# Kernel optimization log

Hardware: AMD Instinct MI355X
Metric: run time of the kernel (lower is better)

Reference implementation:

```python
import jax, jax.numpy as jnp
import numpy as np

H = 8  # num_heads
EPS = 1e-5


def _lin_params(key, din, dout, scale=0.02):
    kw, _ = jax.random.split(key)
    W = jax.random.normal(kw, (din, dout), jnp.float32) * scale
    b = jnp.zeros((dout,), jnp.float32)
    return W, b


def _edge_attention(x_src, x_dst, ei, ea, Wq, bq, Wk, bk, Wv, bv, We, be, Wo, bo, n_dst):
    out_c = Wq.shape[1]
    D = out_c // H
    scale = D ** -0.5
    q = (x_dst @ Wq + bq).reshape(-1, H, D)
    k = (x_src @ Wk + bk).reshape(-1, H, D)
    v = (x_src @ Wv + bv).reshape(-1, H, D)
    e = (ea @ We + be).reshape(-1, H, D)
    src, dst = ei[0], ei[1]
    ke = k[src] + e                                # [E,H,D]
    ve = v[src] + e                                # [E,H,D]
    s = jnp.einsum('ehd,ehd->eh', q[dst], ke) * scale  # [E,H]
    # segment (per-destination) softmax, numerically stable
    m = jax.ops.segment_max(s, dst, num_segments=n_dst)
    ex = jnp.exp(s - m[dst])
    den = jax.ops.segment_sum(ex, dst, num_segments=n_dst)
    a = ex / den[dst]                              # [E,H]  (dropout = identity in eval)
    agg = jax.ops.segment_sum(a[..., None] * ve, dst, num_segments=n_dst)  # [N_dst,H,D]
    return agg.reshape(n_dst, out_c) @ Wo + bo


def _layernorm(x, g, b):
    mu = jnp.mean(x, axis=-1, keepdims=True)
    var = jnp.mean((x - mu) ** 2, axis=-1, keepdims=True)
    return (x - mu) * jax.lax.rsqrt(var + EPS) * g + b


def setup_inputs() -> dict:
    key = jax.random.key(0)
    ks = jax.random.split(key, 32)
    N_pc, N_gr, E_pp, E_pg = 50000, 8000, 400000, 100000
    din, dout, de = 128, 128, 64
    inp = {}
    inp['x_pc'] = jax.random.normal(ks[0], (N_pc, din), jnp.float32)
    inp['x_gr'] = jax.random.normal(ks[1], (N_gr, din), jnp.float32)
    inp['ea_pp'] = jax.random.normal(ks[2], (E_pp, de), jnp.float32)
    inp['ea_pg'] = jax.random.normal(ks[3], (E_pg, de), jnp.float32)
    inp['ei_pp'] = jax.random.randint(ks[4], (2, E_pp), 0, N_pc, jnp.int32)
    src_pg = jax.random.randint(ks[5], (E_pg,), 0, N_pc, jnp.int32)
    dst_pg = jax.random.randint(ks[6], (E_pg,), 0, N_gr, jnp.int32)
    inp['ei_pg'] = jnp.stack([src_pg, dst_pg])
    i = 7
    for et in ('pp', 'pg'):
        for nm, d_in in (('Wq', din), ('Wk', din), ('Wv', din), ('We', de), ('Wo', dout)):
            W, b = _lin_params(ks[i], d_in, dout); i += 1
            inp[f'{nm}_{et}'] = W
            inp[f'b{nm[1].lower()}_{et}'] = b
    for nt, d_in in (('pc', din), ('gr', din)):
        W, b = _lin_params(ks[i], d_in, dout); i += 1
        inp[f'Wnp_{nt}'] = W
        inp[f'bnp_{nt}'] = b
        inp[f'g_{nt}'] = jnp.ones((dout,), jnp.float32)
        inp[f'bln_{nt}'] = jnp.zeros((dout,), jnp.float32)
    return inp


def reference(x_pc, x_gr, ea_pp, ea_pg, ei_pp, ei_pg,
              Wq_pp, bq_pp, Wk_pp, bk_pp, Wv_pp, bv_pp, We_pp, be_pp, Wo_pp, bo_pp,
              Wq_pg, bq_pg, Wk_pg, bk_pg, Wv_pg, bv_pg, We_pg, be_pg, Wo_pg, bo_pg,
              Wnp_pc, bnp_pc, Wnp_gr, bnp_gr, g_pc, bln_pc, g_gr, bln_gr):
    N_pc, N_gr = x_pc.shape[0], x_gr.shape[0]
    out_pc = x_pc @ Wnp_pc + bnp_pc
    out_gr = x_gr @ Wnp_gr + bnp_gr
    out_pc = out_pc + _edge_attention(x_pc, x_pc, ei_pp, ea_pp,
                                      Wq_pp, bq_pp, Wk_pp, bk_pp, Wv_pp, bv_pp,
                                      We_pp, be_pp, Wo_pp, bo_pp, N_pc)
    out_gr = out_gr + _edge_attention(x_pc, x_gr, ei_pg, ea_pg,
                                      Wq_pg, bq_pg, Wk_pg, bk_pg, Wv_pg, bv_pg,
                                      We_pg, be_pg, Wo_pg, bo_pg, N_gr)
    out_pc = _layernorm(out_pc, g_pc, bln_pc)
    out_gr = _layernorm(out_gr, g_gr, bln_gr)
    return out_pc, out_gr
```

## Files before the change

### kernel.cpp

```cpp
#include <hip/hip_runtime.h>
#include <hip/hip_bf16.h>
#include <stdint.h>

typedef short short8 __attribute__((ext_vector_type(8)));
typedef float f32x4 __attribute__((ext_vector_type(4)));

__device__ __forceinline__ unsigned short f2bf(float x) {
    unsigned u = __float_as_uint(x);
    u += 0x7fffu + ((u >> 16) & 1u);
    return (unsigned short)(u >> 16);
}
__device__ __forceinline__ float bflo(unsigned u) { return __uint_as_float(u << 16); }
__device__ __forceinline__ float bfhi(unsigned u) { return __uint_as_float(u & 0xffff0000u); }

struct WDesc { const float* src; unsigned short* dst; int K, ldd, koff, perm; };
struct WPack { WDesc w[12]; };

__global__ __launch_bounds__(256) void prep_and_count(WPack p,
        const int* __restrict__ d0, int E0, int* c0,
        const int* __restrict__ d1, int E1, int* c1, int nPrep) {
    if ((int)blockIdx.x < nPrep) {
        int wi = blockIdx.x >> 2, chunk = blockIdx.x & 3;
        WDesc d = p.w[wi];
        int total = d.K * 128, cs = total >> 2;
        int lo = chunk * cs, hi = lo + cs;
        for (int i = lo + threadIdx.x; i < hi; i += 256) {
            int n = i / d.K, k = i - n * d.K;
            int kk = d.perm ? (2 * (k & 63) + (k >> 6)) : k;
            d.dst[(size_t)n * d.ldd + d.koff + kk] = f2bf(d.src[(size_t)k * 128 + n]);
        }
    } else {
        int t = (blockIdx.x - nPrep) * 256 + threadIdx.x;
        if (t < E0) atomicAdd(&c0[d0[t]], 1);
        else if (t < E0 + E1) atomicAdd(&c1[d1[t - E0]], 1);
    }
}

struct NodeOut { const unsigned short* Wt; const float* bias; unsigned int* out; int ldc, coloff; };
struct NodePack { NodeOut d[5]; int nout; };

__global__ __launch_bounds__(256) void gemm_node(const float* __restrict__ A0, int M0, NodePack p0,
                                                 int B0,
                                                 const float* __restrict__ A1, int M1, NodePack p1) {
    constexpr int K = 128, LDA = 136, LDB = 72, TLD = 133;
    __shared__ __align__(16) unsigned short As[64 * LDA];
    __shared__ __align__(16) unsigned short Bs[128 * LDB];

    const float* A; int M; NodePack dp; int blk;
    if ((int)blockIdx.x < B0) { A = A0; M = M0; dp = p0; blk = blockIdx.x; }
    else { A = A1; M = M1; dp = p1; blk = blockIdx.x - B0; }

    const int tid = threadIdx.x;
    const int rbase = blk * 64;

    for (int slot = tid; slot < 64 * 16; slot += 256) {
        int row = slot >> 4, kg = slot & 15;
        int gr = rbase + row;
        short8 s8 = {0, 0, 0, 0, 0, 0, 0, 0};
        if (gr < M) {
            const float* a = A + (size_t)gr * K + kg * 8;
            float4 f0 = *reinterpret_cast<const float4*>(a);
            float4 f1 = *reinterpret_cast<const float4*>(a + 4);
            s8[0] = (short)f2bf(f0.x); s8[1] = (short)f2bf(f0.y);
            s8[2] = (short)f2bf(f0.z); s8[3] = (short)f2bf(f0.w);
            s8[4] = (short)f2bf(f1.x); s8[5] = (short)f2bf(f1.y);
            s8[6] = (short)f2bf(f1.z); s8[7] = (short)f2bf(f1.w);
        }
        *reinterpret_cast<short8*>(&As[row * LDA + kg * 8]) = s8;
    }

    const int lane = tid & 63, w = tid >> 6;
    const int rb = (w >> 1) * 32, cb = (w & 1) * 64;
    const int qd = lane >> 4, l16 = lane & 15;

    for (int o = 0; o < dp.nout; ++o) {
        NodeOut d = dp.d[o];
        f32x4 acc[2][4];
#pragma unroll
        for (int rt = 0; rt < 2; ++rt)
#pragma unroll
            for (int ct = 0; ct < 4; ++ct) { f32x4 z = {0.f,0.f,0.f,0.f}; acc[rt][ct] = z; }

        for (int kc = 0; kc < K; kc += 64) {
            __syncthreads();
            for (int slot = tid; slot < 128 * 8; slot += 256) {
                int n = slot >> 3, kg = slot & 7;
                *reinterpret_cast<short8*>(&Bs[n * LDB + kg * 8]) =
                    *reinterpret_cast<const short8*>(d.Wt + (size_t)n * K + kc + kg * 8);
            }
            __syncthreads();
#pragma unroll
            for (int ks = 0; ks < 64; ks += 32) {
                short8 af[2], bfr[4];
#pragma unroll
                for (int rt = 0; rt < 2; ++rt)
                    af[rt] = *reinterpret_cast<const short8*>(
                        &As[(rb + rt * 16 + l16) * LDA + kc + ks + qd * 8]);
#pragma unroll
                for (int ct = 0; ct < 4; ++ct)
                    bfr[ct] = *reinterpret_cast<const short8*>(
                        &Bs[(cb + ct * 16 + l16) * LDB + ks + qd * 8]);
#pragma unroll
                for (int rt = 0; rt < 2; ++rt)
#pragma unroll
                    for (int ct = 0; ct < 4; ++ct)
                        acc[rt][ct] = __builtin_amdgcn_mfma_f32_16x16x32_bf16(
                            af[rt], bfr[ct], acc[rt][ct], 0, 0, 0);
            }
        }

        __syncthreads();
        unsigned short* tile = Bs;
#pragma unroll
        for (int ct = 0; ct < 4; ++ct) {
            int col = cb + ct * 16 + l16;
            float bv = d.bias[col];
#pragma unroll
            for (int rt = 0; rt < 2; ++rt)
#pragma unroll
                for (int r = 0; r < 4; ++r)
                    tile[(rb + rt * 16 + qd * 4 + r) * TLD + col] = f2bf(acc[rt][ct][r] + bv);
        }
        __syncthreads();
#pragma unroll
        for (int rep = 0; rep < 4; ++rep) {
            int lrow = (tid >> 4) + rep * 16, seg = tid & 15;
            int gr = rbase + lrow;
            if (gr < M) {
                uint4 pk;
#pragma unroll
                for (int j = 0; j < 4; ++j) {
                    int pcol = seg * 4 + j;
                    unsigned lo16 = tile[lrow * TLD + pcol];
                    unsigned hi16 = tile[lrow * TLD + pcol + 64];
                    ((unsigned*)&pk)[j] = lo16 | (hi16 << 16);
                }
                *reinterpret_cast<uint4*>(&d.out[(size_t)gr * d.ldc + d.coloff + seg * 4]) = pk;
            }
        }
    }
}

struct EdgePack {
    const float* A; const unsigned short* Wt; const float* bias;
    const int* pos; unsigned int* out; int M;
};

__global__ __launch_bounds__(256) void gemm_edge(EdgePack p0, EdgePack p1, int B0) {
    constexpr int K = 64, LDA = 72, LDB = 72, TLD = 133;
    __shared__ __align__(16) unsigned short As[64 * LDA];
    __shared__ __align__(16) unsigned short Bs[128 * LDB];

    EdgePack p; int blk;
    if ((int)blockIdx.x < B0) { p = p0; blk = blockIdx.x; } else { p = p1; blk = blockIdx.x - B0; }

    const int tid = threadIdx.x;
    const int rbase = blk * 64;

    for (int slot = tid; slot < 64 * 8; slot += 256) {
        int row = slot >> 3, kg = slot & 7;
        int gr = rbase + row;
        short8 s8 = {0, 0, 0, 0, 0, 0, 0, 0};
        if (gr < p.M) {
            const float* a = p.A + (size_t)gr * K + kg * 8;
            float4 f0 = *reinterpret_cast<const float4*>(a);
            float4 f1 = *reinterpret_cast<const float4*>(a + 4);
            s8[0] = (short)f2bf(f0.x); s8[1] = (short)f2bf(f0.y);
            s8[2] = (short)f2bf(f0.z); s8[3] = (short)f2bf(f0.w);
            s8[4] = (short)f2bf(f1.x); s8[5] = (short)f2bf(f1.y);
            s8[6] = (short)f2bf(f1.z); s8[7] = (short)f2bf(f1.w);
        }
        *reinterpret_cast<short8*>(&As[row * LDA + kg * 8]) = s8;
    }
    for (int slot = tid; slot < 128 * 8; slot += 256) {
        int n = slot >> 3, kg = slot & 7;
        *reinterpret_cast<short8*>(&Bs[n * LDB + kg * 8]) =
            *reinterpret_cast<const short8*>(p.Wt + (size_t)n * K + kg * 8);
    }
    __syncthreads();

    const int lane = tid & 63, w = tid >> 6;
    const int rb = (w >> 1) * 32, cb = (w & 1) * 64;
    const int qd = lane >> 4, l16 = lane & 15;

    f32x4 acc[2][4];
#pragma unroll
    for (int rt = 0; rt < 2; ++rt)
#pragma unroll
        for (int ct = 0; ct < 4; ++ct) { f32x4 z = {0.f,0.f,0.f,0.f}; acc[rt][ct] = z; }

#pragma unroll
    for (int ks = 0; ks < 64; ks += 32) {
        short8 af[2], bfr[4];
#pragma unroll
        for (int rt = 0; rt < 2; ++rt)
            af[rt] = *reinterpret_cast<const short8*>(&As[(rb + rt * 16 + l16) * LDA + ks + qd * 8]);
#pragma unroll
        for (int ct = 0; ct < 4; ++ct)
            bfr[ct] = *reinterpret_cast<const short8*>(&Bs[(cb + ct * 16 + l16) * LDB + ks + qd * 8]);
#pragma unroll
        for (int rt = 0; rt < 2; ++rt)
#pragma unroll
            for (int ct = 0; ct < 4; ++ct)
                acc[rt][ct] = __builtin_amdgcn_mfma_f32_16x16x32_bf16(
                    af[rt], bfr[ct], acc[rt][ct], 0, 0, 0);
    }

    __syncthreads();
    unsigned short* tile = Bs;
#pragma unroll
    for (int ct = 0; ct < 4; ++ct) {
        int col = cb + ct * 16 + l16;
        float bv = p.bias[col];
#pragma unroll
        for (int rt = 0; rt < 2; ++rt)
#pragma unroll
            for (int r = 0; r < 4; ++r)
                tile[(rb + rt * 16 + qd * 4 + r) * TLD + col] = f2bf(acc[rt][ct][r] + bv);
    }
    __syncthreads();
#pragma unroll
    for (int rep = 0; rep < 4; ++rep) {
        int lrow = (tid >> 4) + rep * 16, seg = tid & 15;
        int gr = rbase + lrow;
        if (gr < p.M) {
            int dpos = p.pos[gr];
            uint4 pk;
#pragma unroll
            for (int j = 0; j < 4; ++j) {
                int pcol = seg * 4 + j;
                unsigned lo16 = tile[lrow * TLD + pcol];
                unsigned hi16 = tile[lrow * TLD + pcol + 64];
                ((unsigned*)&pk)[j] = lo16 | (hi16 << 16);
            }
            *reinterpret_cast<uint4*>(&p.out[(size_t)dpos * 64 + seg * 4]) = pk;
        }
    }
}

struct OutPack {
    const unsigned short* Aagg; const float* Ax;
    const unsigned short* Wt;
    const float *bo, *bnp, *g, *bln; float* out; int M;
};

__global__ __launch_bounds__(256) void gemm_out_ln(OutPack p0, OutPack p1, int B0) {
    constexpr int K = 256, LDA = 264, LDB = 72, FTLD = 132;
    __shared__ __align__(16) char smemA[64 * LDA * 2];
    __shared__ __align__(16) unsigned short Bs[128 * LDB];
    unsigned short* As = (unsigned short*)smemA;

    OutPack p; int blk;
    if ((int)blockIdx.x < B0) { p = p0; blk = blockIdx.x; } else { p = p1; blk = blockIdx.x - B0; }

    const int tid = threadIdx.x;
    const int rbase = blk * 64;

    for (int slot = tid; slot < 64 * 32; slot += 256) {
        int row = slot >> 5, kg = slot & 31;
        int gr = rbase + row;
        short8 s8 = {0, 0, 0, 0, 0, 0, 0, 0};
        if (gr < p.M) {
            if (kg < 16) {
                s8 = *reinterpret_cast<const short8*>(p.Aagg + (size_t)gr * 128 + kg * 8);
            } else {
                const float* a = p.Ax + (size_t)gr * 128 + (kg - 16) * 8;
                float4 f0 = *reinterpret_cast<const float4*>(a);
                float4 f1 = *reinterpret_cast<const float4*>(a + 4);
                s8[0] = (short)f2bf(f0.x); s8[1] = (short)f2bf(f0.y);
                s8[2] = (short)f2bf(f0.z); s8[3] = (short)f2bf(f0.w);
                s8[4] = (short)f2bf(f1.x); s8[5] = (short)f2bf(f1.y);
                s8[6] = (short)f2bf(f1.z); s8[7] = (short)f2bf(f1.w);
            }
        }
        *reinterpret_cast<short8*>(&As[row * LDA + kg * 8]) = s8;
    }

    const int lane = tid & 63, w = tid >> 6;
    const int rb = (w >> 1) * 32, cb = (w & 1) * 64;
    const int qd = lane >> 4, l16 = lane & 15;

    f32x4 acc[2][4];
#pragma unroll
    for (int rt = 0; rt < 2; ++rt)
#pragma unroll
        for (int ct = 0; ct < 4; ++ct) { f32x4 z = {0.f,0.f,0.f,0.f}; acc[rt][ct] = z; }

    for (int kc = 0; kc < K; kc += 64) {
        __syncthreads();
        for (int slot = tid; slot < 128 * 8; slot += 256) {
            int n = slot >> 3, kg = slot & 7;
            *reinterpret_cast<short8*>(&Bs[n * LDB + kg * 8]) =
                *reinterpret_cast<const short8*>(p.Wt + (size_t)n * K + kc + kg * 8);
        }
        __syncthreads();
#pragma unroll
        for (int ks = 0; ks < 64; ks += 32) {
            short8 af[2], bfr[4];
#pragma unroll
            for (int rt = 0; rt < 2; ++rt)
                af[rt] = *reinterpret_cast<const short8*>(
                    &As[(rb + rt * 16 + l16) * LDA + kc + ks + qd * 8]);
#pragma unroll
            for (int ct = 0; ct < 4; ++ct)
                bfr[ct] = *reinterpret_cast<const short8*>(
                    &Bs[(cb + ct * 16 + l16) * LDB + ks + qd * 8]);
#pragma unroll
            for (int rt = 0; rt < 2; ++rt)
#pragma unroll
                for (int ct = 0; ct < 4; ++ct)
                    acc[rt][ct] = __builtin_amdgcn_mfma_f32_16x16x32_bf16(
                        af[rt], bfr[ct], acc[rt][ct], 0, 0, 0);
        }
    }

    __syncthreads();
    float* ftile = (float*)smemA;
#pragma unroll
    for (int ct = 0; ct < 4; ++ct) {
        int col = cb + ct * 16 + l16;
        float bv = p.bo[col] + p.bnp[col];
#pragma unroll
        for (int rt = 0; rt < 2; ++rt)
#pragma unroll
            for (int r = 0; r < 4; ++r)
                ftile[(rb + rt * 16 + qd * 4 + r) * FTLD + col] = acc[rt][ct][r] + bv;
    }
    __syncthreads();

    int r = tid >> 2, q4 = tid & 3;
    const float* rowp = &ftile[r * FTLD + q4 * 32];
    float s = 0.f, sq = 0.f;
#pragma unroll
    for (int j = 0; j < 8; ++j) {
        float4 v = *reinterpret_cast<const float4*>(rowp + j * 4);
        s += v.x + v.y + v.z + v.w;
        sq += v.x * v.x + v.y * v.y + v.z * v.z + v.w * v.w;
    }
    s += __shfl_xor(s, 1, 64);  s += __shfl_xor(s, 2, 64);
    sq += __shfl_xor(sq, 1, 64); sq += __shfl_xor(sq, 2, 64);
    float mu = s * (1.f / 128.f);
    float var = sq * (1.f / 128.f) - mu * mu;
    float rs = rsqrtf(var + 1e-5f);
    int gr = rbase + r;
    if (gr < p.M) {
#pragma unroll
        for (int j = 0; j < 8; ++j) {
            float4 v = *reinterpret_cast<const float4*>(rowp + j * 4);
            int c = q4 * 32 + j * 4;
            float4 gg = *reinterpret_cast<const float4*>(p.g + c);
            float4 bb = *reinterpret_cast<const float4*>(p.bln + c);
            float4 o;
            o.x = (v.x - mu) * rs * gg.x + bb.x;
            o.y = (v.y - mu) * rs * gg.y + bb.y;
            o.z = (v.z - mu) * rs * gg.z + bb.z;
            o.w = (v.w - mu) * rs * gg.w + bb.w;
            *reinterpret_cast<float4*>(&p.out[(size_t)gr * 128 + c]) = o;
        }
    }
}

__global__ __launch_bounds__(1024) void scan_partial(const int* c0, int N0, int* rp0, int* bs0, int B0,
                                                     const int* c1, int N1, int* rp1, int* bs1) {
    __shared__ int wsum[16];
    const int* c; int* rp; int* bs; int N; int blk;
    if ((int)blockIdx.x < B0) { c = c0; rp = rp0; bs = bs0; N = N0; blk = blockIdx.x; }
    else { c = c1; rp = rp1; bs = bs1; N = N1; blk = blockIdx.x - B0; }
    int tid = threadIdx.x, lane = tid & 63, w = tid >> 6;
    int i = blk * 1024 + tid;
    int v = (i < N) ? c[i] : 0;
    int s = v;
#pragma unroll
    for (int off = 1; off < 64; off <<= 1) {
        int t = __shfl_up(s, off, 64);
        if (lane >= off) s += t;
    }
    if (lane == 63) wsum[w] = s;
    __syncthreads();
    if (w == 0 && lane < 16) {
        int ws = wsum[lane];
#pragma unroll
        for (int off = 1; off < 16; off <<= 1) {
            int t = __shfl_up(ws, off, 64);
            if (lane >= off) ws += t;
        }
        wsum[lane] = ws;
    }
    __syncthreads();
    int wexcl = (w == 0) ? 0 : wsum[w - 1];
    if (i < N) rp[i] = wexcl + s - v;
    if (tid == 0) bs[blk] = wsum[15];
}

__global__ __launch_bounds__(128) void scan_mid(const int* bs0, int* off0, int B0, int* rpN0,
                                                const int* bs1, int* off1, int B1, int* rpN1) {
    int w = threadIdx.x >> 6, lane = threadIdx.x & 63;
    const int* bs = w ? bs1 : bs0;
    int* off = w ? off1 : off0;
    int B = w ? B1 : B0;
    int* rpN = w ? rpN1 : rpN0;
    int v = (lane < B) ? bs[lane] : 0;
    int s = v;
#pragma unroll
    for (int o = 1; o < 64; o <<= 1) {
        int t = __shfl_up(s, o, 64);
        if (lane >= o) s += t;
    }
    if (lane < B) off[lane] = s - v;
    int total = __shfl(s, B - 1, 64);
    if (lane == 0) *rpN = total;
}

__global__ __launch_bounds__(1024) void scan_add(int* rp0, int* cur0, const int* off0, int N0, int B0,
                                                 int* rp1, int* cur1, const int* off1, int N1) {
    int* rp; int* cur; const int* off; int N; int blk;
    if ((int)blockIdx.x < B0) { rp = rp0; cur = cur0; off = off0; N = N0; blk = blockIdx.x; }
    else { rp = rp1; cur = cur1; off = off1; N = N1; blk = blockIdx.x - B0; }
    int i = blk * 1024 + threadIdx.x;
    if (i < N) {
        int vv = rp[i] + off[blk];
        rp[i] = vv;
        cur[i] = vv;
    }
}

__global__ __launch_bounds__(256) void scatter_both(
    const int* __restrict__ s0, const int* __restrict__ d0, int E0, int* cur0, int* pos0, int* srcs0,
    const int* __restrict__ s1, const int* __restrict__ d1, int E1, int* cur1, int* pos1, int* srcs1) {
    int t = blockIdx.x * 256 + threadIdx.x;
    if (t < E0) {
        int p = atomicAdd(&cur0[d0[t]], 1);
        pos0[t] = p;
        srcs0[p] = s0[t];
    } else if (t < E0 + E1) {
        int tt = t - E0;
        int p = atomicAdd(&cur1[d1[tt]], 1);
        pos1[tt] = p;
        srcs1[p] = s1[tt];
    }
}

struct AttnPack {
    const unsigned int *q, *kv, *e;
    const int *srcs;
    const int *row_ptr;
    unsigned int* agg; int N;
};

__global__ __launch_bounds__(256) void attn_gather(AttnPack a0, AttnPack a1, int B0) {
    AttnPack a; int blk;
    if ((int)blockIdx.x < B0) { a = a0; blk = blockIdx.x; } else { a = a1; blk = blockIdx.x - B0; }
    int dst = blk * 4 + (threadIdx.x >> 6);
    if (dst >= a.N) return;
    int lane = threadIdx.x & 63;

    unsigned qp = a.q[(size_t)dst * 64 + lane];
    float qlo = bflo(qp), qhi = bfhi(qp);
    int beg = a.row_ptr[dst], end = a.row_ptr[dst + 1];
    float denl = 0.f, denh = 0.f, accl = 0.f, acch = 0.f;

    int sC = a.srcs[beg];
    unsigned kC = a.kv[(size_t)sC * 128 + lane];
    unsigned vC = a.kv[(size_t)sC * 128 + 64 + lane];
    unsigned eC = a.e[(size_t)beg * 64 + lane];

    for (int i = beg; i < end; ++i) {
        int sN = a.srcs[i + 1];
        unsigned kN = a.kv[(size_t)sN * 128 + lane];
        unsigned vN = a.kv[(size_t)sN * 128 + 64 + lane];
        unsigned eN = a.e[(size_t)(i + 1) * 64 + lane];

        float kl = bflo(kC), kh = bfhi(kC);
        float vl = bflo(vC), vh = bfhi(vC);
        float el = bflo(eC), eh = bfhi(eC);
        float pl = qlo * (kl + el), ph = qhi * (kh + eh);
#pragma unroll
        for (int m = 1; m < 16; m <<= 1) {
            pl += __shfl_xor(pl, m, 64);
            ph += __shfl_xor(ph, m, 64);
        }
        float exl = __expf(pl * 0.25f), exh = __expf(ph * 0.25f);
        denl += exl; denh += exh;
        accl += exl * (vl + el);
        acch += exh * (vh + eh);
        kC = kN; vC = vN; eC = eN;
    }
    float ol = denl > 0.f ? accl / denl : 0.f;
    float oh = denh > 0.f ? acch / denh : 0.f;
    a.agg[(size_t)dst * 64 + lane] = (unsigned)f2bf(ol) | ((unsigned)f2bf(oh) << 16);
}

extern "C" void kernel_launch(void* const* d_in, const int* in_sizes, int n_in,
                              void* d_out, int out_size, void* d_ws, size_t ws_size,
                              hipStream_t stream) {
    const float* x_pc  = (const float*)d_in[0];
    const float* x_gr  = (const float*)d_in[1];
    const float* ea_pp = (const float*)d_in[2];
    const float* ea_pg = (const float*)d_in[3];
    const int* ei_pp   = (const int*)d_in[4];
    const int* ei_pg   = (const int*)d_in[5];
    const float *Wq_pp = (const float*)d_in[6],  *bq_pp = (const float*)d_in[7];
    const float *Wk_pp = (const float*)d_in[8],  *bk_pp = (const float*)d_in[9];
    const float *Wv_pp = (const float*)d_in[10], *bv_pp = (const float*)d_in[11];
    const float *We_pp = (const float*)d_in[12], *be_pp = (const float*)d_in[13];
    const float *Wo_pp = (const float*)d_in[14], *bo_pp = (const float*)d_in[15];
    const float *Wq_pg = (const float*)d_in[16], *bq_pg = (const float*)d_in[17];
    const float *Wk_pg = (const float*)d_in[18], *bk_pg = (const float*)d_in[19];
    const float *Wv_pg = (const float*)d_in[20], *bv_pg = (const float*)d_in[21];
    const float *We_pg = (const float*)d_in[22], *be_pg = (const float*)d_in[23];
    const float *Wo_pg = (const float*)d_in[24], *bo_pg = (const float*)d_in[25];
    const float *Wnp_pc = (const float*)d_in[26], *bnp_pc = (const float*)d_in[27];
    const float *g_pc   = (const float*)d_in[28], *bln_pc = (const float*)d_in[29];
    const float *Wnp_gr = (const float*)d_in[30], *bnp_gr = (const float*)d_in[31];
    const float *g_gr   = (const float*)d_in[32], *bln_gr = (const float*)d_in[33];

    const int N_pc = in_sizes[0] / 128;
    const int N_gr = in_sizes[1] / 128;
    const int E_pp = in_sizes[4] / 2;
    const int E_pg = in_sizes[5] / 2;

    char* ws = (char*)d_ws;
    size_t off = 0;
    auto alloc = [&](size_t bytes) -> char* {
        char* p = ws + off;
        off += (bytes + 255) & ~(size_t)255;
        return p;
    };
    unsigned short* Wt_q_pp = (unsigned short*)alloc(128 * 128 * 2);
    unsigned short* Wt_k_pp = (unsigned short*)alloc(128 * 128 * 2);
    unsigned short* Wt_v_pp = (unsigned short*)alloc(128 * 128 * 2);
    unsigned short* Wt_k_pg = (unsigned short*)alloc(128 * 128 * 2);
    unsigned short* Wt_v_pg = (unsigned short*)alloc(128 * 128 * 2);
    unsigned short* Wt_q_pg = (unsigned short*)alloc(128 * 128 * 2);
    unsigned short* Wt_e_pp = (unsigned short*)alloc(64 * 128 * 2);
    unsigned short* Wt_e_pg = (unsigned short*)alloc(64 * 128 * 2);
    unsigned short* Wt_cat_pp = (unsigned short*)alloc(256 * 128 * 2);
    unsigned short* Wt_cat_gr = (unsigned short*)alloc(256 * 128 * 2);

    unsigned int* q_pp  = (unsigned int*)alloc((size_t)N_pc * 64 * 4);
    unsigned int* kv_pp = (unsigned int*)alloc((size_t)N_pc * 128 * 4);
    unsigned int* q_pg  = (unsigned int*)alloc((size_t)N_gr * 64 * 4);
    unsigned int* kv_pg = (unsigned int*)alloc((size_t)N_pc * 128 * 4);
    unsigned int* e_pp  = (unsigned int*)alloc((size_t)(E_pp + 1) * 64 * 4);
    unsigned int* e_pg  = (unsigned int*)alloc((size_t)(E_pg + 1) * 64 * 4);
    unsigned int* agg_pp = (unsigned int*)alloc((size_t)N_pc * 64 * 4);
    unsigned int* agg_pg = (unsigned int*)alloc((size_t)N_gr * 64 * 4);
    int* row_ptr_pp = (int*)alloc((size_t)(N_pc + 1) * 4);
    int* cursor_pp  = (int*)alloc((size_t)N_pc * 4);
    int* pos_pp     = (int*)alloc((size_t)E_pp * 4);
    int* row_ptr_pg = (int*)alloc((size_t)(N_gr + 1) * 4);
    int* cursor_pg  = (int*)alloc((size_t)N_gr * 4);
    int* pos_pg     = (int*)alloc((size_t)E_pg * 4);
    int* bsum_pp    = (int*)alloc(64 * 4);
    int* boff_pp    = (int*)alloc(64 * 4);
    int* bsum_pg    = (int*)alloc(64 * 4);
    int* boff_pg    = (int*)alloc(64 * 4);
    char* zbase = ws + off;
    int* counts_pp = (int*)alloc((size_t)N_pc * 4);
    int* counts_pg = (int*)alloc((size_t)N_gr * 4);
    int* srcs_pp   = (int*)alloc((size_t)(E_pp + 8) * 4);
    int* srcs_pg   = (int*)alloc((size_t)(E_pg + 8) * 4);
    size_t zbytes = (size_t)((ws + off) - zbase);
    hipMemsetAsync(zbase, 0, zbytes, stream);

    float* out_pc = (float*)d_out;
    float* out_gr = out_pc + (size_t)N_pc * 128;

    const int* src_pp = ei_pp;
    const int* dst_pp = ei_pp + E_pp;
    const int* src_pg = ei_pg;
    const int* dst_pg = ei_pg + E_pg;

    WPack wp;
    wp.w[0]  = {Wq_pp, Wt_q_pp, 128, 128, 0, 0};
    wp.w[1]  = {Wk_pp, Wt_k_pp, 128, 128, 0, 0};
    wp.w[2]  = {Wv_pp, Wt_v_pp, 128, 128, 0, 0};
    wp.w[3]  = {Wk_pg, Wt_k_pg, 128, 128, 0, 0};
    wp.w[4]  = {Wv_pg, Wt_v_pg, 128, 128, 0, 0};
    wp.w[5]  = {Wq_pg, Wt_q_pg, 128, 128, 0, 0};
    wp.w[6]  = {We_pp, Wt_e_pp, 64, 64, 0, 0};
    wp.w[7]  = {We_pg, Wt_e_pg, 64, 64, 0, 0};
    wp.w[8]  = {Wo_pp, Wt_cat_pp, 128, 256, 0, 1};
    wp.w[9]  = {Wnp_pc, Wt_cat_pp, 128, 256, 128, 0};
    wp.w[10] = {Wo_pg, Wt_cat_gr, 128, 256, 0, 1};
    wp.w[11] = {Wnp_gr, Wt_cat_gr, 128, 256, 128, 0};
    const int NPREP = 48;
    const int gE = (E_pp + E_pg + 255) / 256;
    prep_and_count<<<NPREP + gE, 256, 0, stream>>>(wp, dst_pp, E_pp, counts_pp,
                                                   dst_pg, E_pg, counts_pg, NPREP);

    const int Bs_pp = (N_pc + 1023) / 1024, Bs_pg = (N_gr + 1023) / 1024;
    scan_partial<<<Bs_pp + Bs_pg, 1024, 0, stream>>>(counts_pp, N_pc, row_ptr_pp, bsum_pp, Bs_pp,
                                                     counts_pg, N_gr, row_ptr_pg, bsum_pg);
    scan_mid<<<1, 128, 0, stream>>>(bsum_pp, boff_pp, Bs_pp, &row_ptr_pp[N_pc],
                                    bsum_pg, boff_pg, Bs_pg, &row_ptr_pg[N_gr]);
    scan_add<<<Bs_pp + Bs_pg, 1024, 0, stream>>>(row_ptr_pp, cursor_pp, boff_pp, N_pc, Bs_pp,
                                                 row_ptr_pg, cursor_pg, boff_pg, N_gr);
    scatter_both<<<gE, 256, 0, stream>>>(src_pp, dst_pp, E_pp, cursor_pp, pos_pp, srcs_pp,
                                         src_pg, dst_pg, E_pg, cursor_pg, pos_pg, srcs_pg);

    NodePack np;
    np.d[0] = {Wt_q_pp, bq_pp, q_pp, 64, 0};
    np.d[1] = {Wt_k_pp, bk_pp, kv_pp, 128, 0};
    np.d[2] = {Wt_v_pp, bv_pp, kv_pp, 128, 64};
    np.d[3] = {Wt_k_pg, bk_pg, kv_pg, 128, 0};
    np.d[4] = {Wt_v_pg, bv_pg, kv_pg, 128, 64};
    np.nout = 5;
    NodePack ng{};
    ng.d[0] = {Wt_q_pg, bq_pg, q_pg, 64, 0};
    ng.nout = 1;
    int Bn0 = (N_pc + 63) / 64, Bn1 = (N_gr + 63) / 64;
    gemm_node<<<Bn0 + Bn1, 256, 0, stream>>>(x_pc, N_pc, np, Bn0, x_gr, N_gr, ng);

    EdgePack ep0 = {ea_pp, Wt_e_pp, be_pp, pos_pp, e_pp, E_pp};
    EdgePack ep1 = {ea_pg, Wt_e_pg, be_pg, pos_pg, e_pg, E_pg};
    int Be0 = (E_pp + 63) / 64, Be1 = (E_pg + 63) / 64;
    gemm_edge<<<Be0 + Be1, 256, 0, stream>>>(ep0, ep1, Be0);

    AttnPack ap0 = {q_pp, kv_pp, e_pp, srcs_pp, row_ptr_pp, agg_pp, N_pc};
    AttnPack ap1 = {q_pg, kv_pg, e_pg, srcs_pg, row_ptr_pg, agg_pg, N_gr};
    int Ba0 = (N_pc + 3) / 4, Ba1 = (N_gr + 3) / 4;
    attn_gather<<<Ba0 + Ba1, 256, 0, stream>>>(ap0, ap1, Ba0);

    OutPack op0 = {(const unsigned short*)agg_pp, x_pc, Wt_cat_pp, bo_pp, bnp_pc, g_pc, bln_pc, out_pc, N_pc};
    OutPack op1 = {(const unsigned short*)agg_pg, x_gr, Wt_cat_gr, bo_pg, bnp_gr, g_gr, bln_gr, out_gr, N_gr};
    int Bo0 = (N_pc + 63) / 64, Bo1 = (N_gr + 63) / 64;
    gemm_out_ln<<<Bo0 + Bo1, 256, 0, stream>>>(op0, op1, Bo0);
}
```

Baseline: 532.8 us.

## Fuse CSR scatter into edge GEMM, single-pass lookback scan, merge node/edge GEMMs

Replaces the three-kernel scan with a single decoupled-lookback scan kernel and drops the separate scatter kernel. The edge GEMM now does the atomic cursor increments itself, keeping positions in shared memory instead of a global pos array. Node and edge GEMMs are merged into one launch, and srcs now stores pre-multiplied offsets so the attention kernel skips that multiply, which also gets vectorised f32x2 math. This cuts launches and global traffic. The risk is that the lookback spin-waits assume all earlier blocks are resident, and atomic ordering makes edge order within each segment nondeterministic.

```diff
diff --git a/kernel.cpp b/kernel.cpp
--- a/kernel.cpp
+++ b/kernel.cpp
@@ -4,14 +4,19 @@
 
 typedef short short8 __attribute__((ext_vector_type(8)));
 typedef float f32x4 __attribute__((ext_vector_type(4)));
+typedef float f32x2 __attribute__((ext_vector_type(2)));
 
 __device__ __forceinline__ unsigned short f2bf(float x) {
     unsigned u = __float_as_uint(x);
     u += 0x7fffu + ((u >> 16) & 1u);
     return (unsigned short)(u >> 16);
 }
-__device__ __forceinline__ float bflo(unsigned u) { return __uint_as_float(u << 16); }
-__device__ __forceinline__ float bfhi(unsigned u) { return __uint_as_float(u & 0xffff0000u); }
+__device__ __forceinline__ f32x2 up2(unsigned u) {
+    f32x2 r;
+    r.x = __uint_as_float(u << 16);
+    r.y = __uint_as_float(u & 0xffff0000u);
+    return r;
+}
 
 struct WDesc { const float* src; unsigned short* dst; int K, ldd, koff, perm; };
 struct WPack { WDesc w[12]; };
@@ -36,85 +41,145 @@
     }
 }
 
+__global__ __launch_bounds__(1024) void scan_lookback(
+        const int* c0, int N0, int* rp0, int* cur0, int B0, int* flg0,
+        const int* c1, int N1, int* rp1, int* cur1, int* flg1) {
+    __shared__ int wsum[16];
+    __shared__ int pref_s;
+    const int* c; int* rp; int* cur; int* flg; int N, blk, B;
+    if ((int)blockIdx.x < B0) { c = c0; rp = rp0; cur = cur0; flg = flg0; N = N0; blk = blockIdx.x; B = B0; }
+    else { c = c1; rp = rp1; cur = cur1; flg = flg1; N = N1; blk = blockIdx.x - B0; B = gridDim.x - B0; }
+    int tid = threadIdx.x, lane = tid & 63, w = tid >> 6;
+    int i = blk * 1024 + tid;
+    int v = (i < N) ? c[i] : 0;
+    int s = v;
+#pragma unroll
+    for (int off = 1; off < 64; off <<= 1) {
+        int t = __shfl_up(s, off, 64);
+        if (lane >= off) s += t;
+    }
+    if (lane == 63) wsum[w] = s;
+    __syncthreads();
+    if (w == 0 && lane < 16) {
+        int ws = wsum[lane];
+#pragma unroll
+        for (int off = 1; off < 16; off <<= 1) {
+            int t = __shfl_up(ws, off, 64);
+            if (lane >= off) ws += t;
+        }
+        wsum[lane] = ws;
+    }
+    __syncthreads();
+    int total = wsum[15];
+    if (tid == 0) atomicExch(&flg[blk], total + 1);
+    if (w == 0) {
+        int mysum = 0;
+        if (lane < blk) {
+            int t;
+            do { t = atomicAdd(&flg[lane], 0); } while (t == 0);
+            mysum = t - 1;
+        }
+#pragma unroll
+        for (int o = 1; o < 64; o <<= 1) mysum += __shfl_xor(mysum, o, 64);
+        if (lane == 0) pref_s = mysum;
+    }
+    __syncthreads();
+    int prefix = pref_s;
+    int wexcl = (w == 0) ? 0 : wsum[w - 1];
+    if (i < N) {
+        int val = prefix + wexcl + (s - v);
+        rp[i] = val;
+        cur[i] = val;
+    }
+    if (blk == B - 1 && tid == 0) rp[N] = prefix + total;
+}
+
 struct NodeOut { const unsigned short* Wt; const float* bias; unsigned int* out; int ldc, coloff; };
 struct NodePack { NodeOut d[5]; int nout; };
-
-__global__ __launch_bounds__(256) void gemm_node(const float* __restrict__ A0, int M0, NodePack p0,
-                                                 int B0,
-                                                 const float* __restrict__ A1, int M1, NodePack p1) {
-    constexpr int K = 128, LDA = 136, LDB = 72, TLD = 133;
-    __shared__ __align__(16) unsigned short As[64 * LDA];
-    __shared__ __align__(16) unsigned short Bs[128 * LDB];
-
-    const float* A; int M; NodePack dp; int blk;
-    if ((int)blockIdx.x < B0) { A = A0; M = M0; dp = p0; blk = blockIdx.x; }
-    else { A = A1; M = M1; dp = p1; blk = blockIdx.x - B0; }
+struct EdgeJob {
+    const float* A; const unsigned short* Wt; const float* bias;
+    const int* srcI; const int* dstI; int* cursor; int* srcs; unsigned int* out; int M;
+};
+
+__global__ __launch_bounds__(256) void gemm_fused(
+        EdgeJob e0, EdgeJob e1, int Be0, int BeTot,
+        const float* An0, int Mn0, NodePack np0, int Bn0,
+        const float* An1, int Mn1, NodePack np1) {
+    __shared__ __align__(16) unsigned short sA[64 * 136];
+    __shared__ __align__(16) unsigned short sB[128 * 72];
+    __shared__ int pos_s[64];
 
     const int tid = threadIdx.x;
-    const int rbase = blk * 64;
-
-    for (int slot = tid; slot < 64 * 16; slot += 256) {
-        int row = slot >> 4, kg = slot & 15;
-        int gr = rbase + row;
-        short8 s8 = {0, 0, 0, 0, 0, 0, 0, 0};
-        if (gr < M) {
-            const float* a = A + (size_t)gr * K + kg * 8;
-            float4 f0 = *reinterpret_cast<const float4*>(a);
-            float4 f1 = *reinterpret_cast<const float4*>(a + 4);
-            s8[0] = (short)f2bf(f0.x); s8[1] = (short)f2bf(f0.y);
-            s8[2] = (short)f2bf(f0.z); s8[3] = (short)f2bf(f0.w);
-            s8[4] = (short)f2bf(f1.x); s8[5] = (short)f2bf(f1.y);
-            s8[6] = (short)f2bf(f1.z); s8[7] = (short)f2bf(f1.w);
-        }
-        *reinterpret_cast<short8*>(&As[row * LDA + kg * 8]) = s8;
-    }
-
     const int lane = tid & 63, w = tid >> 6;
     const int rb = (w >> 1) * 32, cb = (w & 1) * 64;
     const int qd = lane >> 4, l16 = lane & 15;
 
-    for (int o = 0; o < dp.nout; ++o) {
-        NodeOut d = dp.d[o];
+    if ((int)blockIdx.x < BeTot) {
+        constexpr int LDA = 72, LDB = 72, TLD = 133;
+        EdgeJob p; int blk;
+        if ((int)blockIdx.x < Be0) { p = e0; blk = blockIdx.x; }
+        else { p = e1; blk = blockIdx.x - Be0; }
+        const int rbase = blk * 64;
+
+        if (tid < 64) {
+            int t = rbase + tid, pp = 0;
+            if (t < p.M) {
+                int d = p.dstI[t];
+                pp = atomicAdd(&p.cursor[d], 1);
+                p.srcs[pp] = p.srcI[t] * 128;
+            }
+            pos_s[tid] = pp;
+        }
+        for (int slot = tid; slot < 64 * 8; slot += 256) {
+            int row = slot >> 3, kg = slot & 7;
+            int gr = rbase + row;
+            short8 s8 = {0, 0, 0, 0, 0, 0, 0, 0};
+            if (gr < p.M) {
+                const float* a = p.A + (size_t)gr * 64 + kg * 8;
+                float4 f0 = *reinterpret_cast<const float4*>(a);
+                float4 f1 = *reinterpret_cast<const float4*>(a + 4);
+                s8[0] = (short)f2bf(f0.x); s8[1] = (short)f2bf(f0.y);
+                s8[2] = (short)f2bf(f0.z); s8[3] = (short)f2bf(f0.w);
+                s8[4] = (short)f2bf(f1.x); s8[5] = (short)f2bf(f1.y);
+                s8[6] = (short)f2bf(f1.z); s8[7] = (short)f2bf(f1.w);
+            }
+            *reinterpret_cast<short8*>(&sA[row * LDA + kg * 8]) = s8;
+        }
+        for (int slot = tid; slot < 128 * 8; slot += 256) {
+            int n = slot >> 3, kg = slot & 7;
+            *reinterpret_cast<short8*>(&sB[n * LDB + kg * 8]) =
+                *reinterpret_cast<const short8*>(p.Wt + (size_t)n * 64 + kg * 8);
+        }
+        __syncthreads();
+
         f32x4 acc[2][4];
 #pragma unroll
         for (int rt = 0; rt < 2; ++rt)
 #pragma unroll
             for (int ct = 0; ct < 4; ++ct) { f32x4 z = {0.f,0.f,0.f,0.f}; acc[rt][ct] = z; }
-
-        for (int kc = 0; kc < K; kc += 64) {
-            __syncthreads();
-            for (int slot = tid; slot < 128 * 8; slot += 256) {
-                int n = slot >> 3, kg = slot & 7;
-                *reinterpret_cast<short8*>(&Bs[n * LDB + kg * 8]) =
-                    *reinterpret_cast<const short8*>(d.Wt + (size_t)n * K + kc + kg * 8);
-            }
-            __syncthreads();
-#pragma unroll
-            for (int ks = 0; ks < 64; ks += 32) {
-                short8 af[2], bfr[4];
-#pragma unroll
-                for (int rt = 0; rt < 2; ++rt)
-                    af[rt] = *reinterpret_cast<const short8*>(
-                        &As[(rb + rt * 16 + l16) * LDA + kc + ks + qd * 8]);
+#pragma unroll
+        for (int ks = 0; ks < 64; ks += 32) {
+            short8 af[2], bfr[4];
+#pragma unroll
+            for (int rt = 0; rt < 2; ++rt)
+                af[rt] = *reinterpret_cast<const short8*>(&sA[(rb + rt * 16 + l16) * LDA + ks + qd * 8]);
+#pragma unroll
+            for (int ct = 0; ct < 4; ++ct)
+                bfr[ct] = *reinterpret_cast<const short8*>(&sB[(cb + ct * 16 + l16) * LDB + ks + qd * 8]);
+#pragma unroll
+            for (int rt = 0; rt < 2; ++rt)
 #pragma unroll
                 for (int ct = 0; ct < 4; ++ct)
-                    bfr[ct] = *reinterpret_cast<const short8*>(
-                        &Bs[(cb + ct * 16 + l16) * LDB + ks + qd * 8]);
-#pragma unroll
-                for (int rt = 0; rt < 2; ++rt)
-#pragma unroll
-                    for (int ct = 0; ct < 4; ++ct)
-                        acc[rt][ct] = __builtin_amdgcn_mfma_f32_16x16x32_bf16(
-                            af[rt], bfr[ct], acc[rt][ct], 0, 0, 0);
-            }
+                    acc[rt][ct] = __builtin_amdgcn_mfma_f32_16x16x32_bf16(
+                        af[rt], bfr[ct], acc[rt][ct], 0, 0, 0);
         }
 
         __syncthreads();
-        unsigned short* tile = Bs;
+        unsigned short* tile = sB;
 #pragma unroll
         for (int ct = 0; ct < 4; ++ct) {
             int col = cb + ct * 16 + l16;
-            float bv = d.bias[col];
+            float bv = p.bias[col];
 #pragma unroll
             for (int rt = 0; rt < 2; ++rt)
 #pragma unroll
@@ -126,7 +191,8 @@
         for (int rep = 0; rep < 4; ++rep) {
             int lrow = (tid >> 4) + rep * 16, seg = tid & 15;
             int gr = rbase + lrow;
-            if (gr < M) {
+            if (gr < p.M) {
+                int dpos = pos_s[lrow];
                 uint4 pk;
 #pragma unroll
                 for (int j = 0; j < 4; ++j) {
@@ -135,105 +201,98 @@
                     unsigned hi16 = tile[lrow * TLD + pcol + 64];
                     ((unsigned*)&pk)[j] = lo16 | (hi16 << 16);
                 }
-                *reinterpret_cast<uint4*>(&d.out[(size_t)gr * d.ldc + d.coloff + seg * 4]) = pk;
-            }
-        }
-    }
-}
-
-struct EdgePack {
-    const float* A; const unsigned short* Wt; const float* bias;
-    const int* pos; unsigned int* out; int M;
-};
-
-__global__ __launch_bounds__(256) void gemm_edge(EdgePack p0, EdgePack p1, int B0) {
-    constexpr int K = 64, LDA = 72, LDB = 72, TLD = 133;
-    __shared__ __align__(16) unsigned short As[64 * LDA];
-    __shared__ __align__(16) unsigned short Bs[128 * LDB];
-
-    EdgePack p; int blk;
-    if ((int)blockIdx.x < B0) { p = p0; blk = blockIdx.x; } else { p = p1; blk = blockIdx.x - B0; }
-
-    const int tid = threadIdx.x;
-    const int rbase = blk * 64;
-
-    for (int slot = tid; slot < 64 * 8; slot += 256) {
-        int row = slot >> 3, kg = slot & 7;
-        int gr = rbase + row;
-        short8 s8 = {0, 0, 0, 0, 0, 0, 0, 0};
-        if (gr < p.M) {
-            const float* a = p.A + (size_t)gr * K + kg * 8;
-            float4 f0 = *reinterpret_cast<const float4*>(a);
-            float4 f1 = *reinterpret_cast<const float4*>(a + 4);
-            s8[0] = (short)f2bf(f0.x); s8[1] = (short)f2bf(f0.y);
-            s8[2] = (short)f2bf(f0.z); s8[3] = (short)f2bf(f0.w);
-            s8[4] = (short)f2bf(f1.x); s8[5] = (short)f2bf(f1.y);
-            s8[6] = (short)f2bf(f1.z); s8[7] = (short)f2bf(f1.w);
-        }
-        *reinterpret_cast<short8*>(&As[row * LDA + kg * 8]) = s8;
-    }
-    for (int slot = tid; slot < 128 * 8; slot += 256) {
-        int n = slot >> 3, kg = slot & 7;
-        *reinterpret_cast<short8*>(&Bs[n * LDB + kg * 8]) =
-            *reinterpret_cast<const short8*>(p.Wt + (size_t)n * K + kg * 8);
-    }
-    __syncthreads();
-
-    const int lane = tid & 63, w = tid >> 6;
-    const int rb = (w >> 1) * 32, cb = (w & 1) * 64;
-    const int qd = lane >> 4, l16 = lane & 15;
-
-    f32x4 acc[2][4];
-#pragma unroll
-    for (int rt = 0; rt < 2; ++rt)
-#pragma unroll
-        for (int ct = 0; ct < 4; ++ct) { f32x4 z = {0.f,0.f,0.f,0.f}; acc[rt][ct] = z; }
-
-#pragma unroll
-    for (int ks = 0; ks < 64; ks += 32) {
-        short8 af[2], bfr[4];
-#pragma unroll
-        for (int rt = 0; rt < 2; ++rt)
-            af[rt] = *reinterpret_cast<const short8*>(&As[(rb + rt * 16 + l16) * LDA + ks + qd * 8]);
-#pragma unroll
-        for (int ct = 0; ct < 4; ++ct)
-            bfr[ct] = *reinterpret_cast<const short8*>(&Bs[(cb + ct * 16 + l16) * LDB + ks + qd * 8]);
-#pragma unroll
-        for (int rt = 0; rt < 2; ++rt)
-#pragma unroll
-            for (int ct = 0; ct < 4; ++ct)
-                acc[rt][ct] = __builtin_amdgcn_mfma_f32_16x16x32_bf16(
-                    af[rt], bfr[ct], acc[rt][ct], 0, 0, 0);
-    }
-
-    __syncthreads();
-    unsigned short* tile = Bs;
-#pragma unroll
-    for (int ct = 0; ct < 4; ++ct) {
-        int col = cb + ct * 16 + l16;
-        float bv = p.bias[col];
-#pragma unroll
-        for (int rt = 0; rt < 2; ++rt)
-#pragma unroll
-            for (int r = 0; r < 4; ++r)
-                tile[(rb + rt * 16 + qd * 4 + r) * TLD + col] = f2bf(acc[rt][ct][r] + bv);
-    }
-    __syncthreads();
-#pragma unroll
-    for (int rep = 0; rep < 4; ++rep) {
-        int lrow = (tid >> 4) + rep * 16, seg = tid & 15;
-        int gr = rbase + lrow;
-        if (gr < p.M) {
-            int dpos = p.pos[gr];
-            uint4 pk;
-#pragma unroll
-            for (int j = 0; j < 4; ++j) {
-                int pcol = seg * 4 + j;
-                unsigned lo16 = tile[lrow * TLD + pcol];
-                unsigned hi16 = tile[lrow * TLD + pcol + 64];
-                ((unsigned*)&pk)[j] = lo16 | (hi16 << 16);
-            }
-            *reinterpret_cast<uint4*>(&p.out[(size_t)dpos * 64 + seg * 4]) = pk;
+                *reinterpret_cast<uint4*>(&p.out[(size_t)dpos * 64 + seg * 4]) = pk;
+            }
+        }
+    } else {
+        constexpr int LDA = 136, LDB = 72, TLD = 133;
+        int b = blockIdx.x - BeTot;
+        const float* A; int M; NodePack dp; int blk;
+        if (b < Bn0) { A = An0; M = Mn0; dp = np0; blk = b; }
+        else { A = An1; M = Mn1; dp = np1; blk = b - Bn0; }
+        const int rbase = blk * 64;
+
+        for (int slot = tid; slot < 64 * 16; slot += 256) {
+            int row = slot >> 4, kg = slot & 15;
+            int gr = rbase + row;
+            short8 s8 = {0, 0, 0, 0, 0, 0, 0, 0};
+            if (gr < M) {
+                const float* a = A + (size_t)gr * 128 + kg * 8;
+                float4 f0 = *reinterpret_cast<const float4*>(a);
+                float4 f1 = *reinterpret_cast<const float4*>(a + 4);
+                s8[0] = (short)f2bf(f0.x); s8[1] = (short)f2bf(f0.y);
+                s8[2] = (short)f2bf(f0.z); s8[3] = (short)f2bf(f0.w);
+                s8[4] = (short)f2bf(f1.x); s8[5] = (short)f2bf(f1.y);
+                s8[6] = (short)f2bf(f1.z); s8[7] = (short)f2bf(f1.w);
+            }
+            *reinterpret_cast<short8*>(&sA[row * LDA + kg * 8]) = s8;
+        }
+
+        for (int o = 0; o < dp.nout; ++o) {
+            NodeOut d = dp.d[o];
+            f32x4 acc[2][4];
+#pragma unroll
+            for (int rt = 0; rt < 2; ++rt)
+#pragma unroll
+                for (int ct = 0; ct < 4; ++ct) { f32x4 z = {0.f,0.f,0.f,0.f}; acc[rt][ct] = z; }
+
+            for (int kc = 0; kc < 128; kc += 64) {
+                __syncthreads();
+                for (int slot = tid; slot < 128 * 8; slot += 256) {
+                    int n = slot >> 3, kg = slot & 7;
+                    *reinterpret_cast<short8*>(&sB[n * LDB + kg * 8]) =
+                        *reinterpret_cast<const short8*>(d.Wt + (size_t)n * 128 + kc + kg * 8);
+                }
+                __syncthreads();
+#pragma unroll
+                for (int ks = 0; ks < 64; ks += 32) {
+                    short8 af[2], bfr[4];
+#pragma unroll
+                    for (int rt = 0; rt < 2; ++rt)
+                        af[rt] = *reinterpret_cast<const short8*>(
+                            &sA[(rb + rt * 16 + l16) * LDA + kc + ks + qd * 8]);
+#pragma unroll
+                    for (int ct = 0; ct < 4; ++ct)
+                        bfr[ct] = *reinterpret_cast<const short8*>(
+                            &sB[(cb + ct * 16 + l16) * LDB + ks + qd * 8]);
+#pragma unroll
+                    for (int rt = 0; rt < 2; ++rt)
+#pragma unroll
+                        for (int ct = 0; ct < 4; ++ct)
+                            acc[rt][ct] = __builtin_amdgcn_mfma_f32_16x16x32_bf16(
+                                af[rt], bfr[ct], acc[rt][ct], 0, 0, 0);
+                }
+            }
+
+            __syncthreads();
+            unsigned short* tile = sB;
+#pragma unroll
+            for (int ct = 0; ct < 4; ++ct) {
+                int col = cb + ct * 16 + l16;
+                float bv = d.bias[col];
+#pragma unroll
+                for (int rt = 0; rt < 2; ++rt)
+#pragma unroll
+                    for (int r = 0; r < 4; ++r)
+                        tile[(rb + rt * 16 + qd * 4 + r) * TLD + col] = f2bf(acc[rt][ct][r] + bv);
+            }
+            __syncthreads();
+#pragma unroll
+            for (int rep = 0; rep < 4; ++rep) {
+                int lrow = (tid >> 4) + rep * 16, seg = tid & 15;
+                int gr = rbase + lrow;
+                if (gr < M) {
+                    uint4 pk;
+#pragma unroll
+                    for (int j = 0; j < 4; ++j) {
+                        int pcol = seg * 4 + j;
+                        unsigned lo16 = tile[lrow * TLD + pcol];
+                        unsigned hi16 = tile[lrow * TLD + pcol + 64];
+                        ((unsigned*)&pk)[j] = lo16 | (hi16 << 16);
+                    }
+                    *reinterpret_cast<uint4*>(&d.out[(size_t)gr * d.ldc + d.coloff + seg * 4]) = pk;
+                }
+            }
         }
     }
 }
@@ -360,86 +419,6 @@
     }
 }
 
-__global__ __launch_bounds__(1024) void scan_partial(const int* c0, int N0, int* rp0, int* bs0, int B0,
-                                                     const int* c1, int N1, int* rp1, int* bs1) {
-    __shared__ int wsum[16];
-    const int* c; int* rp; int* bs; int N; int blk;
-    if ((int)blockIdx.x < B0) { c = c0; rp = rp0; bs = bs0; N = N0; blk = blockIdx.x; }
-    else { c = c1; rp = rp1; bs = bs1; N = N1; blk = blockIdx.x - B0; }
-    int tid = threadIdx.x, lane = tid & 63, w = tid >> 6;
-    int i = blk * 1024 + tid;
-    int v = (i < N) ? c[i] : 0;
-    int s = v;
-#pragma unroll
-    for (int off = 1; off < 64; off <<= 1) {
-        int t = __shfl_up(s, off, 64);
-        if (lane >= off) s += t;
-    }
-    if (lane == 63) wsum[w] = s;
-    __syncthreads();
-    if (w == 0 && lane < 16) {
-        int ws = wsum[lane];
-#pragma unroll
-        for (int off = 1; off < 16; off <<= 1) {
-            int t = __shfl_up(ws, off, 64);
-            if (lane >= off) ws += t;
-        }
-        wsum[lane] = ws;
-    }
-    __syncthreads();
-    int wexcl = (w == 0) ? 0 : wsum[w - 1];
-    if (i < N) rp[i] = wexcl + s - v;
-    if (tid == 0) bs[blk] = wsum[15];
-}
-
-__global__ __launch_bounds__(128) void scan_mid(const int* bs0, int* off0, int B0, int* rpN0,
-                                                const int* bs1, int* off1, int B1, int* rpN1) {
-    int w = threadIdx.x >> 6, lane = threadIdx.x & 63;
-    const int* bs = w ? bs1 : bs0;
-    int* off = w ? off1 : off0;
-    int B = w ? B1 : B0;
-    int* rpN = w ? rpN1 : rpN0;
-    int v = (lane < B) ? bs[lane] : 0;
-    int s = v;
-#pragma unroll
-    for (int o = 1; o < 64; o <<= 1) {
-        int t = __shfl_up(s, o, 64);
-        if (lane >= o) s += t;
-    }
-    if (lane < B) off[lane] = s - v;
-    int total = __shfl(s, B - 1, 64);
-    if (lane == 0) *rpN = total;
-}
-
-__global__ __launch_bounds__(1024) void scan_add(int* rp0, int* cur0, const int* off0, int N0, int B0,
-                                                 int* rp1, int* cur1, const int* off1, int N1) {
-    int* rp; int* cur; const int* off; int N; int blk;
-    if ((int)blockIdx.x < B0) { rp = rp0; cur = cur0; off = off0; N = N0; blk = blockIdx.x; }
-    else { rp = rp1; cur = cur1; off = off1; N = N1; blk = blockIdx.x - B0; }
-    int i = blk * 1024 + threadIdx.x;
-    if (i < N) {
-        int vv = rp[i] + off[blk];
-        rp[i] = vv;
-        cur[i] = vv;
-    }
-}
-
-__global__ __launch_bounds__(256) void scatter_both(
-    const int* __restrict__ s0, const int* __restrict__ d0, int E0, int* cur0, int* pos0, int* srcs0,
-    const int* __restrict__ s1, const int* __restrict__ d1, int E1, int* cur1, int* pos1, int* srcs1) {
-    int t = blockIdx.x * 256 + threadIdx.x;
-    if (t < E0) {
-        int p = atomicAdd(&cur0[d0[t]], 1);
-        pos0[t] = p;
-        srcs0[p] = s0[t];
-    } else if (t < E0 + E1) {
-        int tt = t - E0;
-        int p = atomicAdd(&cur1[d1[tt]], 1);
-        pos1[tt] = p;
-        srcs1[p] = s1[tt];
-    }
-}
-
 struct AttnPack {
     const unsigned int *q, *kv, *e;
     const int *srcs;
@@ -454,39 +433,38 @@
     if (dst >= a.N) return;
     int lane = threadIdx.x & 63;
 
-    unsigned qp = a.q[(size_t)dst * 64 + lane];
-    float qlo = bflo(qp), qhi = bfhi(qp);
+    f32x2 q2 = up2(a.q[(size_t)dst * 64 + lane]);
     int beg = a.row_ptr[dst], end = a.row_ptr[dst + 1];
-    float denl = 0.f, denh = 0.f, accl = 0.f, acch = 0.f;
-
-    int sC = a.srcs[beg];
-    unsigned kC = a.kv[(size_t)sC * 128 + lane];
-    unsigned vC = a.kv[(size_t)sC * 128 + 64 + lane];
+    f32x2 den = {0.f, 0.f}, acc = {0.f, 0.f};
+
+    int oC = a.srcs[beg];
+    unsigned kC = a.kv[oC + lane];
+    unsigned vC = a.kv[oC + 64 + lane];
     unsigned eC = a.e[(size_t)beg * 64 + lane];
 
     for (int i = beg; i < end; ++i) {
-        int sN = a.srcs[i + 1];
-        unsigned kN = a.kv[(size_t)sN * 128 + lane];
-        unsigned vN = a.kv[(size_t)sN * 128 + 64 + lane];
+        int oN = a.srcs[i + 1];
+        unsigned kN = a.kv[oN + lane];
+        unsigned vN = a.kv[oN + 64 + lane];
         unsigned eN = a.e[(size_t)(i + 1) * 64 + lane];
 
-        float kl = bflo(kC), kh = bfhi(kC);
-        float vl = bflo(vC), vh = bfhi(vC);
-        float el = bflo(eC), eh = bfhi(eC);
-        float pl = qlo * (kl + el), ph = qhi * (kh + eh);
+        f32x2 kk = up2(kC), vv = up2(vC), ee = up2(eC);
+        f32x2 ke = kk + ee;
+        float pl = q2.x * ke.x, ph = q2.y * ke.y;
 #pragma unroll
         for (int m = 1; m < 16; m <<= 1) {
             pl += __shfl_xor(pl, m, 64);
             ph += __shfl_xor(ph, m, 64);
         }
-        float exl = __expf(pl * 0.25f), exh = __expf(ph * 0.25f);
-        denl += exl; denh += exh;
-        accl += exl * (vl + el);
-        acch += exh * (vh + eh);
+        f32x2 ex;
+        ex.x = __expf(pl * 0.25f);
+        ex.y = __expf(ph * 0.25f);
+        den += ex;
+        acc += ex * (vv + ee);
         kC = kN; vC = vN; eC = eN;
     }
-    float ol = denl > 0.f ? accl / denl : 0.f;
-    float oh = denh > 0.f ? acch / denh : 0.f;
+    float ol = den.x > 0.f ? acc.x / den.x : 0.f;
+    float oh = den.y > 0.f ? acc.y / den.y : 0.f;
     a.agg[(size_t)dst * 64 + lane] = (unsigned)f2bf(ol) | ((unsigned)f2bf(oh) << 16);
 }
 
@@ -547,17 +525,13 @@
     unsigned int* agg_pg = (unsigned int*)alloc((size_t)N_gr * 64 * 4);
     int* row_ptr_pp = (int*)alloc((size_t)(N_pc + 1) * 4);
     int* cursor_pp  = (int*)alloc((size_t)N_pc * 4);
-    int* pos_pp     = (int*)alloc((size_t)E_pp * 4);
     int* row_ptr_pg = (int*)alloc((size_t)(N_gr + 1) * 4);
     int* cursor_pg  = (int*)alloc((size_t)N_gr * 4);
-    int* pos_pg     = (int*)alloc((size_t)E_pg * 4);
-    int* bsum_pp    = (int*)alloc(64 * 4);
-    int* boff_pp    = (int*)alloc(64 * 4);
-    int* bsum_pg    = (int*)alloc(64 * 4);
-    int* boff_pg    = (int*)alloc(64 * 4);
     char* zbase = ws + off;
     int* counts_pp = (int*)alloc((size_t)N_pc * 4);
     int* counts_pg = (int*)alloc((size_t)N_gr * 4);
+    int* flg_pp    = (int*)alloc(64 * 4);
+    int* flg_pg    = (int*)alloc(64 * 4);
     int* srcs_pp   = (int*)alloc((size_t)(E_pp + 8) * 4);
     int* srcs_pg   = (int*)alloc((size_t)(E_pg + 8) * 4);
     size_t zbytes = (size_t)((ws + off) - zbase);
@@ -590,15 +564,13 @@
                                                    dst_pg, E_pg, counts_pg, NPREP);
 
     const int Bs_pp = (N_pc + 1023) / 1024, Bs_pg = (N_gr + 1023) / 1024;
-    scan_partial<<<Bs_pp + Bs_pg, 1024, 0, stream>>>(counts_pp, N_pc, row_ptr_pp, bsum_pp, Bs_pp,
-                                                     counts_pg, N_gr, row_ptr_pg, bsum_pg);
-    scan_mid<<<1, 128, 0, stream>>>(bsum_pp, boff_pp, Bs_pp, &row_ptr_pp[N_pc],
-                                    bsum_pg, boff_pg, Bs_pg, &row_ptr_pg[N_gr]);
-    scan_add<<<Bs_pp + Bs_pg, 1024, 0, stream>>>(row_ptr_pp, cursor_pp, boff_pp, N_pc, Bs_pp,
-                                                 row_ptr_pg, cursor_pg, boff_pg, N_gr);
-    scatter_both<<<gE, 256, 0, stream>>>(src_pp, dst_pp, E_pp, cursor_pp, pos_pp, srcs_pp,
-                                         src_pg, dst_pg, E_pg, cursor_pg, pos_pg, srcs_pg);
-
+    scan_lookback<<<Bs_pp + Bs_pg, 1024, 0, stream>>>(
+        counts_pp, N_pc, row_ptr_pp, cursor_pp, Bs_pp, flg_pp,
+        counts_pg, N_gr, row_ptr_pg, cursor_pg, flg_pg);
+
+    EdgeJob ej0 = {ea_pp, Wt_e_pp, be_pp, src_pp, dst_pp, cursor_pp, srcs_pp, e_pp, E_pp};
+    EdgeJob ej1 = {ea_pg, Wt_e_pg, be_pg, src_pg, dst_pg, cursor_pg, srcs_pg, e_pg, E_pg};
+    int Be0 = (E_pp + 63) / 64, Be1 = (E_pg + 63) / 64;
     NodePack np;
     np.d[0] = {Wt_q_pp, bq_pp, q_pp, 64, 0};
     np.d[1] = {Wt_k_pp, bk_pp, kv_pp, 128, 0};
@@ -610,12 +582,8 @@
     ng.d[0] = {Wt_q_pg, bq_pg, q_pg, 64, 0};
     ng.nout = 1;
     int Bn0 = (N_pc + 63) / 64, Bn1 = (N_gr + 63) / 64;
-    gemm_node<<<Bn0 + Bn1, 256, 0, stream>>>(x_pc, N_pc, np, Bn0, x_gr, N_gr, ng);
-
-    EdgePack ep0 = {ea_pp, Wt_e_pp, be_pp, pos_pp, e_pp, E_pp};
-    EdgePack ep1 = {ea_pg, Wt_e_pg, be_pg, pos_pg, e_pg, E_pg};
-    int Be0 = (E_pp + 63) / 64, Be1 = (E_pg + 63) / 64;
-    gemm_edge<<<Be0 + Be1, 256, 0, stream>>>(ep0, ep1, Be0);
+    gemm_fused<<<Be0 + Be1 + Bn0 + Bn1, 256, 0, stream>>>(
+        ej0, ej1, Be0, Be0 + Be1, x_pc, N_pc, np, Bn0, x_gr, N_gr, ng);
 
     AttnPack ap0 = {q_pp, kv_pp, e_pp, srcs_pp, row_ptr_pp, agg_pp, N_pc};
     AttnPack ap1 = {q_pg, kv_pg, e_pg, srcs_pg, row_ptr_pg, agg_pg, N_gr};
```

Result: no change. 541.4 us (+1.6%).
